# Kernel tuning notes

Hardware: AMD Instinct MI355X
Metric: run time of the kernel (lower is better)

Reference implementation:

```python
import jax, jax.numpy as jnp
import numpy as np

D = 4096

def setup_inputs() -> dict:
    key = jax.random.key(0)
    k1, k2 = jax.random.split(key)
    matrix = jax.random.normal(k1, (D, D), dtype=jnp.float32)
    n = jax.random.normal(k2, (D,), dtype=jnp.float32)
    return {"matrix": matrix, "n": n}

def reference(matrix, n):
    # matrix @ matrix.T is PSD; adding a strictly positive softplus diagonal makes it SPD
    m = matrix @ matrix.T + jnp.diag(jax.nn.softplus(n))
    return jnp.linalg.cholesky(m)
```

## Files before the change

kernel.cpp:

```cpp
#include <hip/hip_runtime.h>
#include <math.h>

#define D 4096
#define NB 128
#define TSY 128
#define KC 32
#define NTILES (D / TSY)
#define LDP 40

typedef __attribute__((ext_vector_type(8))) short short8;
typedef __attribute__((ext_vector_type(4))) float f32x4;
typedef __attribute__((ext_vector_type(4))) unsigned int uint4v;
typedef unsigned short ush;

__device__ __forceinline__ float softplusf(float x) {
  return fmaxf(x, 0.0f) + log1pf(expf(-fabsf(x)));
}

struct HL { unsigned int h, l; };

__device__ __forceinline__ HL split2(float x0, float x1) {
  unsigned int b0 = __float_as_uint(x0), b1 = __float_as_uint(x1);
  unsigned int h0 = b0 & 0xFFFF0000u, h1 = b1 & 0xFFFF0000u;
  float r0 = x0 - __uint_as_float(h0);
  float r1 = x1 - __uint_as_float(h1);
  HL out;
  out.h = h1 | (h0 >> 16);
  out.l = (__float_as_uint(r1) & 0xFFFF0000u) | (__float_as_uint(r0) >> 16);
  return out;
}

__device__ void potrf_factor(float (*Ls)[NB + 1]) {
  int tid = threadIdx.x;
  int lane = tid & 63, wid = tid >> 6;
  int tx = tid & 15, ty = tid >> 4;

  for (int pp = 0; pp < 8; ++pp) {
    int pc0 = pp * 16;
    if (wid == 0) {
      int ra = lane, rb = lane + 64;
      bool va = (ra >= pc0), vb = (rb >= pc0);
      float xa[16], xb[16];
#pragma unroll
      for (int c = 0; c < 16; ++c) {
        xa[c] = va ? Ls[ra][pc0 + c] : 0.0f;
        xb[c] = vb ? Ls[rb][pc0 + c] : 0.0f;
      }
#pragma unroll
      for (int j = 0; j < 16; ++j) {
        int jj = pc0 + j;
        float dv = (jj < 64) ? __shfl(xa[j], jj) : __shfl(xb[j], jj - 64);
        float s = 1.0f / sqrtf(dv);
        xa[j] *= s;
        xb[j] *= s;
        float mja = (ra > jj) ? xa[j] : 0.0f;
        float mjb = (rb > jj) ? xb[j] : 0.0f;
#pragma unroll
        for (int c = j + 1; c < 16; ++c) {
          int rc = pc0 + c;
          float lc = (rc < 64) ? __shfl(xa[j], rc) : __shfl(xb[j], rc - 64);
          xa[c] -= mja * lc;
          xb[c] -= mjb * lc;
        }
      }
      if (va) {
#pragma unroll
        for (int c = 0; c < 16; ++c) Ls[ra][pc0 + c] = xa[c];
      }
      if (vb) {
#pragma unroll
        for (int c = 0; c < 16; ++c) Ls[rb][pc0 + c] = xb[c];
      }
    }
    __syncthreads();

    int s0 = pc0 + 16;
    if (s0 < NB) {
      int r0 = ty * 8, c0 = tx * 8;
      if (r0 >= s0 && c0 >= s0) {
        float acc[8][8];
#pragma unroll
        for (int rr = 0; rr < 8; ++rr) {
          float4 m0 = *(const float4*)&Ls[r0 + rr][c0];
          float4 m1 = *(const float4*)&Ls[r0 + rr][c0 + 4];
          acc[rr][0] = m0.x; acc[rr][1] = m0.y; acc[rr][2] = m0.z; acc[rr][3] = m0.w;
          acc[rr][4] = m1.x; acc[rr][5] = m1.y; acc[rr][6] = m1.z; acc[rr][7] = m1.w;
        }
#pragma unroll
        for (int q = 0; q < 16; ++q) {
          float av[8], bv[8];
#pragma unroll
          for (int rr = 0; rr < 8; ++rr) av[rr] = Ls[r0 + rr][pc0 + q];
#pragma unroll
          for (int cc = 0; cc < 8; ++cc) bv[cc] = Ls[c0 + cc][pc0 + q];
#pragma unroll
          for (int rr = 0; rr < 8; ++rr)
#pragma unroll
            for (int cc = 0; cc < 8; ++cc) acc[rr][cc] -= av[rr] * bv[cc];
        }
#pragma unroll
        for (int rr = 0; rr < 8; ++rr) {
          *(float4*)&Ls[r0 + rr][c0] =
              make_float4(acc[rr][0], acc[rr][1], acc[rr][2], acc[rr][3]);
          *(float4*)&Ls[r0 + rr][c0 + 4] =
              make_float4(acc[rr][4], acc[rr][5], acc[rr][6], acc[rr][7]);
        }
      }
    }
    __syncthreads();
  }
}

__device__ void potrf_store(float* Msrc, float (*Ls)[NB + 1]) {
  int tid = threadIdx.x;
  for (int idx = tid; idx < NB * NB; idx += 256) {
    int i = idx >> 7, j = idx & (NB - 1);
    Msrc[(size_t)i * D + j] = (j <= i) ? Ls[i][j] : 0.0f;
  }
}

__global__ __launch_bounds__(256) void syrk0_kernel(
    const float* __restrict__ Asrc, const float* __restrict__ nvec,
    float* __restrict__ Mout)
{
  __shared__ __align__(16) unsigned char smem[66560];
  ush (*Ah)[LDP] = (ush(*)[LDP])(smem);
  ush (*Al)[LDP] = (ush(*)[LDP])(smem + 10240);
  ush (*Bh)[LDP] = (ush(*)[LDP])(smem + 20480);
  ush (*Bl)[LDP] = (ush(*)[LDP])(smem + 30720);
  float (*Ls)[NB + 1] = (float(*)[NB + 1])smem;

  int b = blockIdx.x;
  int ti = (int)((sqrtf(8.0f * (float)b + 1.0f) - 1.0f) * 0.5f);
  while ((ti + 1) * (ti + 2) / 2 <= b) ++ti;
  while (ti * (ti + 1) / 2 > b) --ti;
  int tj = b - ti * (ti + 1) / 2;
  int row0 = ti * TSY, col0 = tj * TSY;

  int tid = threadIdx.x;
  int lane = tid & 63, wid = tid >> 6;
  int wr = wid >> 1, wc = wid & 1;
  int srow = tid >> 1;
  int scg = (tid & 1) * 16;

  f32x4 acc[4][4];
#pragma unroll
  for (int m = 0; m < 4; ++m)
#pragma unroll
    for (int n = 0; n < 4; ++n) acc[m][n] = (f32x4){0.f, 0.f, 0.f, 0.f};

  int lr16 = lane & 15, kof = (lane >> 4) * 8;

  for (int kk = 0; kk < D; kk += KC) {
    const float* pa = Asrc + (size_t)(row0 + srow) * D + kk + scg;
    const float* pb = Asrc + (size_t)(col0 + srow) * D + kk + scg;
    float4 av0 = *(const float4*)(pa + 0), av1 = *(const float4*)(pa + 4);
    float4 av2 = *(const float4*)(pa + 8), av3 = *(const float4*)(pa + 12);
    float4 bv0 = *(const float4*)(pb + 0), bv1 = *(const float4*)(pb + 4);
    float4 bv2 = *(const float4*)(pb + 8), bv3 = *(const float4*)(pb + 12);

    __syncthreads();
    {
      HL p0 = split2(av0.x, av0.y), p1 = split2(av0.z, av0.w);
      HL p2 = split2(av1.x, av1.y), p3 = split2(av1.z, av1.w);
      HL p4 = split2(av2.x, av2.y), p5 = split2(av2.z, av2.w);
      HL p6 = split2(av3.x, av3.y), p7 = split2(av3.z, av3.w);
      uint4v h0 = {p0.h, p1.h, p2.h, p3.h}, l0 = {p0.l, p1.l, p2.l, p3.l};
      uint4v h1 = {p4.h, p5.h, p6.h, p7.h}, l1 = {p4.l, p5.l, p6.l, p7.l};
      *(uint4v*)&Ah[srow][scg] = h0;  *(uint4v*)&Ah[srow][scg + 8] = h1;
      *(uint4v*)&Al[srow][scg] = l0;  *(uint4v*)&Al[srow][scg + 8] = l1;
    }
    {
      HL p0 = split2(bv0.x, bv0.y), p1 = split2(bv0.z, bv0.w);
      HL p2 = split2(bv1.x, bv1.y), p3 = split2(bv1.z, bv1.w);
      HL p4 = split2(bv2.x, bv2.y), p5 = split2(bv2.z, bv2.w);
      HL p6 = split2(bv3.x, bv3.y), p7 = split2(bv3.z, bv3.w);
      uint4v h0 = {p0.h, p1.h, p2.h, p3.h}, l0 = {p0.l, p1.l, p2.l, p3.l};
      uint4v h1 = {p4.h, p5.h, p6.h, p7.h}, l1 = {p4.l, p5.l, p6.l, p7.l};
      *(uint4v*)&Bh[srow][scg] = h0;  *(uint4v*)&Bh[srow][scg + 8] = h1;
      *(uint4v*)&Bl[srow][scg] = l0;  *(uint4v*)&Bl[srow][scg + 8] = l1;
    }
    __syncthreads();

    short8 ah[4], al[4], bh[4], bl[4];
#pragma unroll
    for (int m = 0; m < 4; ++m) {
      int r = wr * 64 + m * 16 + lr16;
      ah[m] = *(const short8*)&Ah[r][kof];
      al[m] = *(const short8*)&Al[r][kof];
    }
#pragma unroll
    for (int n = 0; n < 4; ++n) {
      int c = wc * 64 + n * 16 + lr16;
      bh[n] = *(const short8*)&Bh[c][kof];
      bl[n] = *(const short8*)&Bl[c][kof];
    }
#pragma unroll
    for (int m = 0; m < 4; ++m)
#pragma unroll
      for (int n = 0; n < 4; ++n) {
        acc[m][n] = __builtin_amdgcn_mfma_f32_16x16x32_bf16(ah[m], bh[n], acc[m][n], 0, 0, 0);
        acc[m][n] = __builtin_amdgcn_mfma_f32_16x16x32_bf16(ah[m], bl[n], acc[m][n], 0, 0, 0);
        acc[m][n] = __builtin_amdgcn_mfma_f32_16x16x32_bf16(al[m], bh[n], acc[m][n], 0, 0, 0);
      }
  }

  int cl = lane & 15, rg = (lane >> 4) * 4;

  if (b == 0) {
    __syncthreads();
#pragma unroll
    for (int m = 0; m < 4; ++m)
#pragma unroll
      for (int n = 0; n < 4; ++n) {
        int li0 = wr * 64 + m * 16 + rg;
        int lj = wc * 64 + n * 16 + cl;
#pragma unroll
        for (int r = 0; r < 4; ++r) {
          int li = li0 + r;
          float v = acc[m][n][r];
          if (li == lj) v += softplusf(nvec[li]);
          Ls[li][lj] = v;
        }
      }
    __syncthreads();
    potrf_factor(Ls);
    potrf_store(Mout, Ls);
    return;
  }

#pragma unroll
  for (int m = 0; m < 4; ++m) {
#pragma unroll
    for (int n = 0; n < 4; ++n) {
      int gi0 = row0 + wr * 64 + m * 16 + rg;
      int gj = col0 + wc * 64 + n * 16 + cl;
#pragma unroll
      for (int r = 0; r < 4; ++r) {
        int gi = gi0 + r;
        float v = acc[m][n][r];
        if (gi == gj) v += softplusf(nvec[gi]);
        Mout[(size_t)gi * D + gj] = v;
      }
    }
  }

  if (ti > tj) {
    float4 z = make_float4(0.f, 0.f, 0.f, 0.f);
    int zr = tid >> 1;
    int zc0 = (tid & 1) * 64;
    float* zp = Mout + (size_t)(col0 + zr) * D + row0 + zc0;
#pragma unroll
    for (int q = 0; q < 16; ++q) *(float4*)(zp + 4 * q) = z;
  }
}

__global__ __launch_bounds__(256) void syrk1_kernel(float* __restrict__ M, int kb)
{
  __shared__ __align__(16) unsigned char smem[66560];
  ush (*Ah)[LDP] = (ush(*)[LDP])(smem);
  ush (*Al)[LDP] = (ush(*)[LDP])(smem + 10240);
  ush (*Bh)[LDP] = (ush(*)[LDP])(smem + 20480);
  ush (*Bl)[LDP] = (ush(*)[LDP])(smem + 30720);
  float (*Ls)[NB + 1] = (float(*)[NB + 1])smem;

  const float* Asrc = M + (size_t)(kb + NB) * D + kb;
  float* Mout = M + (size_t)(kb + NB) * D + (kb + NB);

  int s = blockIdx.x;
  int ti = (int)((sqrtf(8.0f * (float)s + 1.0f) - 1.0f) * 0.5f);
  while ((ti + 1) * (ti + 2) / 2 <= s) ++ti;
  while (ti * (ti + 1) / 2 > s) --ti;
  int tj = s - ti * (ti + 1) / 2;
  int row0 = ti * TSY, col0 = tj * TSY;

  int tid = threadIdx.x;
  int lane = tid & 63, wid = tid >> 6;
  int wr = wid >> 1, wc = wid & 1;
  int srow = tid >> 1;
  int scg = (tid & 1) * 16;
  int lr16 = lane & 15, kof = (lane >> 4) * 8;
  int cl = lane & 15, rg = (lane >> 4) * 4;

  f32x4 acc[4][4];
#pragma unroll
  for (int m = 0; m < 4; ++m)
#pragma unroll
    for (int n = 0; n < 4; ++n) acc[m][n] = (f32x4){0.f, 0.f, 0.f, 0.f};

  for (int kk = 0; kk < NB; kk += KC) {
    const float* pa = Asrc + (size_t)(row0 + srow) * D + kk + scg;
    const float* pb = Asrc + (size_t)(col0 + srow) * D + kk + scg;
    float4 av0 = *(const float4*)(pa + 0), av1 = *(const float4*)(pa + 4);
    float4 av2 = *(const float4*)(pa + 8), av3 = *(const float4*)(pa + 12);
    float4 bv0 = *(const float4*)(pb + 0), bv1 = *(const float4*)(pb + 4);
    float4 bv2 = *(const float4*)(pb + 8), bv3 = *(const float4*)(pb + 12);

    __syncthreads();
    {
      HL p0 = split2(av0.x, av0.y), p1 = split2(av0.z, av0.w);
      HL p2 = split2(av1.x, av1.y), p3 = split2(av1.z, av1.w);
      HL p4 = split2(av2.x, av2.y), p5 = split2(av2.z, av2.w);
      HL p6 = split2(av3.x, av3.y), p7 = split2(av3.z, av3.w);
      uint4v h0 = {p0.h, p1.h, p2.h, p3.h}, l0 = {p0.l, p1.l, p2.l, p3.l};
      uint4v h1 = {p4.h, p5.h, p6.h, p7.h}, l1 = {p4.l, p5.l, p6.l, p7.l};
      *(uint4v*)&Ah[srow][scg] = h0;  *(uint4v*)&Ah[srow][scg + 8] = h1;
      *(uint4v*)&Al[srow][scg] = l0;  *(uint4v*)&Al[srow][scg + 8] = l1;
    }
    {
      HL p0 = split2(bv0.x, bv0.y), p1 = split2(bv0.z, bv0.w);
      HL p2 = split2(bv1.x, bv1.y), p3 = split2(bv1.z, bv1.w);
      HL p4 = split2(bv2.x, bv2.y), p5 = split2(bv2.z, bv2.w);
      HL p6 = split2(bv3.x, bv3.y), p7 = split2(bv3.z, bv3.w);
      uint4v h0 = {p0.h, p1.h, p2.h, p3.h}, l0 = {p0.l, p1.l, p2.l, p3.l};
      uint4v h1 = {p4.h, p5.h, p6.h, p7.h}, l1 = {p4.l, p5.l, p6.l, p7.l};
      *(uint4v*)&Bh[srow][scg] = h0;  *(uint4v*)&Bh[srow][scg + 8] = h1;
      *(uint4v*)&Bl[srow][scg] = l0;  *(uint4v*)&Bl[srow][scg + 8] = l1;
    }
    __syncthreads();

    short8 ah[4], al[4], bh[4], bl[4];
#pragma unroll
    for (int m = 0; m < 4; ++m) {
      int r = wr * 64 + m * 16 + lr16;
      ah[m] = *(const short8*)&Ah[r][kof];
      al[m] = *(const short8*)&Al[r][kof];
    }
#pragma unroll
    for (int n = 0; n < 4; ++n) {
      int c = wc * 64 + n * 16 + lr16;
      bh[n] = *(const short8*)&Bh[c][kof];
      bl[n] = *(const short8*)&Bl[c][kof];
    }
#pragma unroll
    for (int m = 0; m < 4; ++m)
#pragma unroll
      for (int n = 0; n < 4; ++n) {
        acc[m][n] = __builtin_amdgcn_mfma_f32_16x16x32_bf16(ah[m], bh[n], acc[m][n], 0, 0, 0);
        acc[m][n] = __builtin_amdgcn_mfma_f32_16x16x32_bf16(ah[m], bl[n], acc[m][n], 0, 0, 0);
        acc[m][n] = __builtin_amdgcn_mfma_f32_16x16x32_bf16(al[m], bh[n], acc[m][n], 0, 0, 0);
      }
  }

  if (s == 0) {
    __syncthreads();
#pragma unroll
    for (int m = 0; m < 4; ++m)
#pragma unroll
      for (int n = 0; n < 4; ++n) {
        int li0 = wr * 64 + m * 16 + rg;
        int lj = wc * 64 + n * 16 + cl;
#pragma unroll
        for (int r = 0; r < 4; ++r) {
          int li = li0 + r;
          Ls[li][lj] = Mout[(size_t)li * D + lj] - acc[m][n][r];
        }
      }
    __syncthreads();
    potrf_factor(Ls);
    potrf_store(Mout, Ls);
    return;
  }

#pragma unroll
  for (int m = 0; m < 4; ++m) {
#pragma unroll
    for (int n = 0; n < 4; ++n) {
      int gi0 = row0 + wr * 64 + m * 16 + rg;
      int gj = col0 + wc * 64 + n * 16 + cl;
#pragma unroll
      for (int r = 0; r < 4; ++r) {
        int gi = gi0 + r;
        Mout[(size_t)gi * D + gj] -= acc[m][n][r];
      }
    }
  }
}

__global__ __launch_bounds__(256) void trsm_kernel(float* __restrict__ M, int kb)
{
  __shared__ float Ls[NB][NB + 1];
  __shared__ float dinv[NB];
  int tid = threadIdx.x;
  const float* Lsrc = M + (size_t)kb * D + kb;
  for (int idx = tid; idx < NB * NB; idx += 256) {
    int i = idx >> 7, j = idx & (NB - 1);
    Ls[i][j] = (j <= i) ? Lsrc[(size_t)i * D + j] : 0.0f;
  }
  __syncthreads();
  if (tid < NB) dinv[tid] = 1.0f / Ls[tid][tid];
  __syncthreads();
  int lane = tid & 63, w = tid >> 6;
  size_t r0 = (size_t)(kb + NB) + (size_t)blockIdx.x * 8 + w * 2;
  float* p0 = M + r0 * D + kb;
  float* p1 = p0 + D;
  float x0l = p0[lane], x0h = p0[64 + lane];
  float x1l = p1[lane], x1h = p1[64 + lane];
  for (int p = 0; p < 64; ++p) {
    float dv = dinv[p];
    float xp0 = __shfl(x0l, p) * dv;
    float xp1 = __shfl(x1l, p) * dv;
    float Llo = Ls[lane][p];
    float Lhi = Ls[64 + lane][p];
    if (lane == p)      { x0l = xp0; x1l = xp1; }
    else if (lane > p)  { x0l -= xp0 * Llo; x1l -= xp1 * Llo; }
    x0h -= xp0 * Lhi;
    x1h -= xp1 * Lhi;
  }
  for (int p = 64; p < NB; ++p) {
    int q = p - 64;
    float dv = dinv[p];
    float xp0 = __shfl(x0h, q) * dv;
    float xp1 = __shfl(x1h, q) * dv;
    float Lhi = Ls[64 + lane][p];
    if (lane == q)      { x0h = xp0; x1h = xp1; }
    else if (lane > q)  { x0h -= xp0 * Lhi; x1h -= xp1 * Lhi; }
  }
  p0[lane] = x0l; p0[64 + lane] = x0h;
  p1[lane] = x1l; p1[64 + lane] = x1h;
}

extern "C" void kernel_launch(void* const* d_in, const int* in_sizes, int n_in,
                              void* d_out, int out_size, void* d_ws, size_t ws_size,
                              hipStream_t stream)
{
  (void)in_sizes; (void)n_in; (void)d_ws; (void)ws_size; (void)out_size;
  const float* A  = (const float*)d_in[0];
  const float* nv = (const float*)d_in[1];
  float* M = (float*)d_out;

  syrk0_kernel<<<NTILES * (NTILES + 1) / 2, 256, 0, stream>>>(A, nv, M);

  for (int k = 0; k <= 30; ++k) {
    int kb = k * NB;
    int T = D - kb - NB;
    int t = T / TSY;
    trsm_kernel<<<T / 8, 256, 0, stream>>>(M, kb);
    syrk1_kernel<<<t * (t + 1) / 2, 256, 0, stream>>>(M, kb);
  }
}
```

Measured before the change: 4.600 ms.

## Split first-panel POTRF into its own kernel and defer diagonal scaling

Moves the first diagonal-block factorization out of syrk0_kernel into a separate single-block potrf_kernel. This shrinks syrk0's shared memory from 66.5KB to about 40KB, which may let more blocks fit per CU. The in-wave panel factorization now uses a reciprocal of the diagonal to form the update multipliers and applies the rsqrt column scaling in a separate pass afterwards. It also switches to the fast rcp/rsq intrinsics, at some cost in precision, and adds one more kernel launch plus an extra global round trip for the 128x128 block.

```diff
diff --git a/kernel.cpp b/kernel.cpp
--- a/kernel.cpp
+++ b/kernel.cpp
@@ -50,18 +50,24 @@
       for (int j = 0; j < 16; ++j) {
         int jj = pc0 + j;
         float dv = (jj < 64) ? __shfl(xa[j], jj) : __shfl(xb[j], jj - 64);
-        float s = 1.0f / sqrtf(dv);
-        xa[j] *= s;
-        xb[j] *= s;
-        float mja = (ra > jj) ? xa[j] : 0.0f;
-        float mjb = (rb > jj) ? xb[j] : 0.0f;
+        float di = __builtin_amdgcn_rcpf(dv);
+        float ta = (ra > jj) ? xa[j] * di : 0.0f;
+        float tb = (rb > jj) ? xb[j] * di : 0.0f;
 #pragma unroll
         for (int c = j + 1; c < 16; ++c) {
           int rc = pc0 + c;
           float lc = (rc < 64) ? __shfl(xa[j], rc) : __shfl(xb[j], rc - 64);
-          xa[c] -= mja * lc;
-          xb[c] -= mjb * lc;
+          xa[c] -= ta * lc;
+          xb[c] -= tb * lc;
         }
+      }
+#pragma unroll
+      for (int c = 0; c < 16; ++c) {
+        int rc = pc0 + c;
+        float dc = (rc < 64) ? __shfl(xa[c], rc) : __shfl(xb[c], rc - 64);
+        float sc = __builtin_amdgcn_rsqf(dc);
+        xa[c] *= sc;
+        xb[c] *= sc;
       }
       if (va) {
 #pragma unroll
@@ -119,16 +125,26 @@
   }
 }
 
+__global__ __launch_bounds__(256) void potrf_kernel(float* __restrict__ M, int kb)
+{
+  __shared__ float Ls[NB][NB + 1];
+  int tid = threadIdx.x;
+  float* Msrc = M + (size_t)kb * D + kb;
+  for (int idx = tid; idx < NB * NB; idx += 256) {
+    int i = idx >> 7, j = idx & (NB - 1);
+    Ls[i][j] = Msrc[(size_t)i * D + j];
+  }
+  __syncthreads();
+  potrf_factor(Ls);
+  potrf_store(Msrc, Ls);
+}
+
 __global__ __launch_bounds__(256) void syrk0_kernel(
     const float* __restrict__ Asrc, const float* __restrict__ nvec,
     float* __restrict__ Mout)
 {
-  __shared__ __align__(16) unsigned char smem[66560];
-  ush (*Ah)[LDP] = (ush(*)[LDP])(smem);
-  ush (*Al)[LDP] = (ush(*)[LDP])(smem + 10240);
-  ush (*Bh)[LDP] = (ush(*)[LDP])(smem + 20480);
-  ush (*Bl)[LDP] = (ush(*)[LDP])(smem + 30720);
-  float (*Ls)[NB + 1] = (float(*)[NB + 1])smem;
+  __shared__ ush Ah[TSY][LDP], Al[TSY][LDP];
+  __shared__ ush Bh[TSY][LDP], Bl[TSY][LDP];
 
   int b = blockIdx.x;
   int ti = (int)((sqrtf(8.0f * (float)b + 1.0f) - 1.0f) * 0.5f);
@@ -206,29 +222,6 @@
   }
 
   int cl = lane & 15, rg = (lane >> 4) * 4;
-
-  if (b == 0) {
-    __syncthreads();
-#pragma unroll
-    for (int m = 0; m < 4; ++m)
-#pragma unroll
-      for (int n = 0; n < 4; ++n) {
-        int li0 = wr * 64 + m * 16 + rg;
-        int lj = wc * 64 + n * 16 + cl;
-#pragma unroll
-        for (int r = 0; r < 4; ++r) {
-          int li = li0 + r;
-          float v = acc[m][n][r];
-          if (li == lj) v += softplusf(nvec[li]);
-          Ls[li][lj] = v;
-        }
-      }
-    __syncthreads();
-    potrf_factor(Ls);
-    potrf_store(Mout, Ls);
-    return;
-  }
-
 #pragma unroll
   for (int m = 0; m < 4; ++m) {
 #pragma unroll
@@ -430,6 +423,7 @@
   float* M = (float*)d_out;
 
   syrk0_kernel<<<NTILES * (NTILES + 1) / 2, 256, 0, stream>>>(A, nv, M);
+  potrf_kernel<<<1, 256, 0, stream>>>(M, 0);
 
   for (int k = 0; k <= 30; ++k) {
     int kb = k * NB;
```

Result: faster. 4.342 ms (-5.6%).
